# Optimization experiments

Measured on AMD Instinct MI355X. Metric: run time of the kernel, lower is better.

## Reference

```python
import jax, jax.numpy as jnp
import numpy as np

B, T, V, E, H, K = 64, 1024, 50000, 128, 256, 20
HD = H // 2  # hidden per LSTM direction


def _p(key, i, shape, scale=0.05):
    return jax.random.normal(jax.random.fold_in(key, i), shape, dtype=jnp.float32) * scale


def setup_inputs():
    key = jax.random.key(0)
    k1, k2, k3 = jax.random.split(key, 3)
    lengths = jax.random.randint(k2, (B,), T // 4, T + 1)
    mask = jnp.arange(T)[None, :] < lengths[:, None]  # [B,T] bool, left-aligned
    x = jax.random.randint(k1, (B, T), 1, V)
    x = jnp.where(mask, x, 0).astype(jnp.int32)  # pad_idx = 0
    tags = jax.random.randint(k3, (B, T), 0, K).astype(jnp.int32)
    inp = {"x": x, "tags": tags, "mask": mask}
    pk = jax.random.key(1)
    inp["emb"] = _p(pk, 0, (V, E)).at[0].set(0.0)  # padding_idx row zeroed
    dims = [E, H]  # layer-1 input is concat of both directions = H
    i = 1
    for l in range(2):
        for suf in ["", "_rev"]:
            inp[f"w_ih_l{l}{suf}"] = _p(pk, i, (4 * HD, dims[l])); i += 1
            inp[f"w_hh_l{l}{suf}"] = _p(pk, i, (4 * HD, HD)); i += 1
            inp[f"b_ih_l{l}{suf}"] = _p(pk, i, (4 * HD,)); i += 1
            inp[f"b_hh_l{l}{suf}"] = _p(pk, i, (4 * HD,)); i += 1
    inp["ln_g"] = jnp.ones((H,), jnp.float32)
    inp["ln_b"] = jnp.zeros((H,), jnp.float32)
    inp["attn_w"] = _p(pk, i, (1, H)); i += 1
    inp["attn_b"] = _p(pk, i, (1,)); i += 1
    inp["fc1_w"] = _p(pk, i, (H, H)); i += 1
    inp["fc1_b"] = _p(pk, i, (H,)); i += 1
    inp["fc2_w"] = _p(pk, i, (K, H)); i += 1
    inp["fc2_b"] = _p(pk, i, (K,)); i += 1
    inp["crf_start"] = _p(pk, i, (K,)); i += 1
    inp["crf_end"] = _p(pk, i, (K,)); i += 1
    inp["crf_trans"] = _p(pk, i, (K, K)); i += 1
    return inp


def _lstm_dir(x, w_ih, w_hh, b_ih, b_hh, reverse):
    # x: [B,T,D] -> [B,T,HD]; torch gate order i,f,g,o
    xs = jnp.swapaxes(x, 0, 1)  # [T,B,D]
    pre = xs @ w_ih.T + b_ih + b_hh  # input contribution precomputed (GEMM)

    def step(carry, g_in):
        h, c = carry
        g = g_in + h @ w_hh.T
        i, f, gc, o = jnp.split(g, 4, axis=-1)
        c = jax.nn.sigmoid(f) * c + jax.nn.sigmoid(i) * jnp.tanh(gc)
        h = jax.nn.sigmoid(o) * jnp.tanh(c)
        return (h, c), h

    nB, nH = x.shape[0], w_hh.shape[1]
    init = (jnp.zeros((nB, nH), x.dtype), jnp.zeros((nB, nH), x.dtype))
    _, hs = jax.lax.scan(step, init, pre, reverse=reverse)
    return jnp.swapaxes(hs, 0, 1)


def _crf_nll(emissions, tags, mask, start, end, trans):
    # torchcrf: llh = score - logZ, reduction='sum'; module returns -llh.mean() (scalar)
    maskf = mask.astype(emissions.dtype)
    em_sc = jnp.take_along_axis(emissions, tags[..., None], axis=2)[..., 0]  # [B,T]
    tr_sc = trans[tags[:, :-1], tags[:, 1:]]  # [B,T-1]
    num = start[tags[:, 0]] + em_sc[:, 0] + jnp.sum(maskf[:, 1:] * (tr_sc + em_sc[:, 1:]), axis=1)
    last = jnp.sum(mask.astype(jnp.int32), axis=1) - 1
    last_tags = jnp.take_along_axis(tags, last[:, None], axis=1)[:, 0]
    num = num + end[last_tags]
    alpha0 = start[None, :] + emissions[:, 0]  # [B,K]
    em_t = jnp.swapaxes(emissions[:, 1:], 0, 1)  # [T-1,B,K]
    m_t = jnp.swapaxes(mask[:, 1:], 0, 1)  # [T-1,B]

    def step(alpha, inp):
        e, m = inp
        nxt = jax.scipy.special.logsumexp(alpha[:, :, None] + trans[None] + e[:, None, :], axis=1)
        return jnp.where(m[:, None], nxt, alpha), None

    alpha, _ = jax.lax.scan(step, alpha0, (em_t, m_t))
    logZ = jax.scipy.special.logsumexp(alpha + end[None, :], axis=1)
    return -jnp.sum(num - logZ)


def reference(x, tags, mask, emb,
              w_ih_l0, w_hh_l0, b_ih_l0, b_hh_l0,
              w_ih_l0_rev, w_hh_l0_rev, b_ih_l0_rev, b_hh_l0_rev,
              w_ih_l1, w_hh_l1, b_ih_l1, b_hh_l1,
              w_ih_l1_rev, w_hh_l1_rev, b_ih_l1_rev, b_hh_l1_rev,
              ln_g, ln_b, attn_w, attn_b, fc1_w, fc1_b, fc2_w, fc2_b,
              crf_start, crf_end, crf_trans):
    mask = mask.at[:, 0].set(True)
    h = emb[x]  # [B,T,E]
    # 2-layer bidirectional LSTM (eval mode: dropout = identity)
    h = jnp.concatenate([
        _lstm_dir(h, w_ih_l0, w_hh_l0, b_ih_l0, b_hh_l0, False),
        _lstm_dir(h, w_ih_l0_rev, w_hh_l0_rev, b_ih_l0_rev, b_hh_l0_rev, True)], axis=-1)
    h = jnp.concatenate([
        _lstm_dir(h, w_ih_l1, w_hh_l1, b_ih_l1, b_hh_l1, False),
        _lstm_dir(h, w_ih_l1_rev, w_hh_l1_rev, b_ih_l1_rev, b_hh_l1_rev, True)], axis=-1)
    # LayerNorm (eps=1e-5)
    mu = jnp.mean(h, axis=-1, keepdims=True)
    var = jnp.mean(jnp.square(h - mu), axis=-1, keepdims=True)
    h = (h - mu) * jax.lax.rsqrt(var + 1e-5) * ln_g + ln_b
    # masked attention + residual broadcast of context
    scores = (h @ attn_w.T)[..., 0] + attn_b[0]  # [B,T]
    scores = jnp.where(mask, scores, jnp.float32(-1e9))
    w = jax.nn.softmax(scores, axis=1)[..., None]  # [B,T,1]
    h = h + jnp.sum(h * w, axis=1, keepdims=True)
    # hidden_fc: Linear + ReLU (dropout identity in eval)
    h = jax.nn.relu(h @ fc1_w.T + fc1_b)
    emissions = h @ fc2_w.T + fc2_b  # [B,T,K]
    return _crf_nll(emissions, tags, mask, crf_start, crf_end, crf_trans)
```

## Files before the change

kernel.cpp:

```cpp
#include <hip/hip_runtime.h>
#include <stdint.h>

#define BB 64
#define TT 1024
#define EE 128

typedef __bf16 bf16x8 __attribute__((ext_vector_type(8)));
typedef float f32x4 __attribute__((ext_vector_type(4)));

#define MFMA16 __builtin_amdgcn_mfma_f32_16x16x32_bf16

__device__ __forceinline__ float bf2f(unsigned short u) {
  union { unsigned int i; float f; } v; v.i = ((unsigned int)u) << 16; return v.f;
}
__device__ __forceinline__ unsigned short f2bf(float f) {
  union { float f; unsigned int i; } v; v.f = f;
  return (unsigned short)((v.i + 0x7fffu + ((v.i >> 16) & 1u)) >> 16);
}
__device__ __forceinline__ float sigf(float x) {
  return __builtin_amdgcn_rcpf(1.f + __expf(-x));
}
__device__ __forceinline__ float tanhf_(float x) {
  return fmaf(2.f, __builtin_amdgcn_rcpf(1.f + __expf(-2.f * x)), -1.f);
}


__global__ __launch_bounds__(256) void cvtbf4(const float* __restrict__ s,
                                              unsigned short* __restrict__ d, int n4) {
  int i = blockIdx.x * 256 + threadIdx.x;
  if (i < n4) {
    float4 v = *(const float4*)&s[(size_t)i * 4];
    ushort4 o; o.x = f2bf(v.x); o.y = f2bf(v.y); o.z = f2bf(v.z); o.w = f2bf(v.w);
    *(ushort4*)&d[(size_t)i * 4] = o;
  }
}

__global__ __launch_bounds__(256) void bias_comb(const float* bi, const float* bh,
                                                 const float* bir, const float* bhr,
                                                 float* __restrict__ o) {
  int j = blockIdx.x * 256 + threadIdx.x;
  if (j < 1024) o[j] = (j < 512) ? (bi[j] + bh[j]) : (bir[j - 512] + bhr[j - 512]);
}

__global__ __launch_bounds__(256) void embed_k(const int* __restrict__ x,
                                               const float* __restrict__ emb,
                                               unsigned short* __restrict__ xe) {
  int i = blockIdx.x * 256 + threadIdx.x;
  int bt = i >> 5, e4 = (i & 31) << 2;
  float4 v = *(const float4*)&emb[(size_t)x[bt] * EE + e4];
  ushort4 o; o.x = f2bf(v.x); o.y = f2bf(v.y); o.z = f2bf(v.z); o.w = f2bf(v.w);
  *(ushort4*)&xe[(size_t)bt * EE + e4] = o;
}


template <bool RELU, bool REMAP>
__global__ __launch_bounds__(256) void gemm_bt(const unsigned short* __restrict__ A,
                                               const unsigned short* __restrict__ W,
                                               const float* __restrict__ bias,
                                               unsigned short* __restrict__ out,
                                               int M, int N, int K) {
  __shared__ unsigned short As[64][40];
  __shared__ unsigned short Ws[64][40];
  const int tid = threadIdx.x, wave = tid >> 6, lane = tid & 63;
  const int m0 = blockIdx.x * 64, n0 = blockIdx.y * 64;
  f32x4 acc[4] = {{0,0,0,0},{0,0,0,0},{0,0,0,0},{0,0,0,0}};
  const int r = tid >> 2, kc = (tid & 3) << 3;
  const int fr = lane & 15, kk = (lane >> 4) << 3;

  for (int k0 = 0; k0 < K; k0 += 32) {
    uint4 av = *(const uint4*)&A[(size_t)(m0 + r) * K + k0 + kc];
    uint4 wv = *(const uint4*)&W[(size_t)(n0 + r) * K + k0 + kc];
    *(uint4*)&As[r][kc] = av;
    *(uint4*)&Ws[r][kc] = wv;
    __syncthreads();
    bf16x8 af = *(const bf16x8*)&As[wave * 16 + fr][kk];
#pragma unroll
    for (int nt = 0; nt < 4; nt++) {
      bf16x8 bv = *(const bf16x8*)&Ws[nt * 16 + fr][kk];
      acc[nt] = MFMA16(af, bv, acc[nt], 0, 0, 0);
    }
    __syncthreads();
  }
  const int cr = (lane >> 4) << 2, cc = lane & 15;
#pragma unroll
  for (int nt = 0; nt < 4; nt++) {
    int gn = n0 + nt * 16 + cc;
    float bs = bias[gn];
#pragma unroll
    for (int rr = 0; rr < 4; rr++) {
      int gm = m0 + wave * 16 + cr + rr;
      float v = acc[nt][rr] + bs;
      if (RELU) v = fmaxf(v, 0.f);
      size_t off;
      if (REMAP) { int b = gm >> 10, t = gm & 1023; off = ((size_t)(t * 64 + b)) * N + gn; }
      else       { off = (size_t)gm * N + gn; }
      out[off] = f2bf(v);
    }
  }
}


__global__ __launch_bounds__(512) void lstm_scan8(const unsigned short* __restrict__ pre,
                                                  const unsigned short* __restrict__ whhb,
                                                  unsigned short* __restrict__ hout) {
  const int b = blockIdx.x, dir = blockIdx.y;
  const int tid = threadIdx.x;
  const int w = tid >> 6, lane = tid & 63;
  const int fr = lane & 15, q = lane >> 4;
  const int u = 16 * w + fr;
  const unsigned short* wb = whhb + (size_t)dir * 65536;

  bf16x8 af[4][4];
#pragma unroll
  for (int G = 0; G < 4; G++)
#pragma unroll
    for (int kt = 0; kt < 4; kt++)
      af[G][kt] = *(const bf16x8*)&wb[(size_t)(128 * G + 16 * w + fr) * 128 + kt * 32 + q * 8];
  asm volatile("" : "+v"(af[0][0]), "+v"(af[0][1]), "+v"(af[0][2]), "+v"(af[0][3]),
                    "+v"(af[1][0]), "+v"(af[1][1]), "+v"(af[1][2]), "+v"(af[1][3]),
                    "+v"(af[2][0]), "+v"(af[2][1]), "+v"(af[2][2]), "+v"(af[2][3]),
                    "+v"(af[3][0]), "+v"(af[3][1]), "+v"(af[3][2]), "+v"(af[3][3]));

  __shared__ alignas(16) unsigned short hS[2][128];
  if (tid < 128) { hS[0][tid] = 0; hS[1][tid] = 0; }

  const int t0 = dir ? 1023 : 0, st = dir ? -1 : 1;
  float c = 0.f;
  const unsigned short* pb = pre + (size_t)b * 1024 + dir * 512 + u;
  unsigned short* hob = hout + (size_t)b * 1024 * 256 + dir * 128 + u;

  unsigned short pg0, pg1, pg2, pg3;
  {
    size_t tb = (size_t)t0 * 65536;
    pg0 = pb[tb]; pg1 = pb[tb + 128]; pg2 = pb[tb + 256]; pg3 = pb[tb + 384];
  }
  __syncthreads();

  int p = 0;
  for (int s = 0; s < 1024; s++) {
    const int t = t0 + st * s;
    bf16x8 bv0 = *(const bf16x8*)&hS[p][q * 8];
    bf16x8 bv1 = *(const bf16x8*)&hS[p][32 + q * 8];
    bf16x8 bv2 = *(const bf16x8*)&hS[p][64 + q * 8];
    bf16x8 bv3 = *(const bf16x8*)&hS[p][96 + q * 8];
    f32x4 c0 = {0,0,0,0}, c1 = {0,0,0,0}, c2 = {0,0,0,0}, c3 = {0,0,0,0};
    c0 = MFMA16(bv0, af[0][0], c0, 0,0,0); c1 = MFMA16(bv0, af[1][0], c1, 0,0,0);
    c2 = MFMA16(bv0, af[2][0], c2, 0,0,0); c3 = MFMA16(bv0, af[3][0], c3, 0,0,0);
    c0 = MFMA16(bv1, af[0][1], c0, 0,0,0); c1 = MFMA16(bv1, af[1][1], c1, 0,0,0);
    c2 = MFMA16(bv1, af[2][1], c2, 0,0,0); c3 = MFMA16(bv1, af[3][1], c3, 0,0,0);
    c0 = MFMA16(bv2, af[0][2], c0, 0,0,0); c1 = MFMA16(bv2, af[1][2], c1, 0,0,0);
    c2 = MFMA16(bv2, af[2][2], c2, 0,0,0); c3 = MFMA16(bv2, af[3][2], c3, 0,0,0);
    c0 = MFMA16(bv3, af[0][3], c0, 0,0,0); c1 = MFMA16(bv3, af[1][3], c1, 0,0,0);
    c2 = MFMA16(bv3, af[2][3], c2, 0,0,0); c3 = MFMA16(bv3, af[3][3], c3, 0,0,0);

    unsigned short ng0 = 0, ng1 = 0, ng2 = 0, ng3 = 0;
    if (s + 1 < 1024) {
      size_t tb = (size_t)(t + st) * 65536;
      ng0 = pb[tb]; ng1 = pb[tb + 128]; ng2 = pb[tb + 256]; ng3 = pb[tb + 384];
    }

    float gi = c0[0] + bf2f(pg0);
    float gf = c1[0] + bf2f(pg1);
    float gg = c2[0] + bf2f(pg2);
    float go = c3[0] + bf2f(pg3);
    float cn = sigf(gf) * c + sigf(gi) * tanhf_(gg);
    c = cn;
    float h = sigf(go) * tanhf_(cn);
    pg0 = ng0; pg1 = ng1; pg2 = ng2; pg3 = ng3;
    unsigned short hb = f2bf(h);
    if (q == 0) {
      hS[p ^ 1][u] = hb;
      hob[(size_t)t * 256] = hb;
    }
    asm volatile("s_waitcnt lgkmcnt(0)\n\ts_barrier" ::: "memory");
    p ^= 1;
  }
}


__global__ __launch_bounds__(256) void ln_attn(const unsigned short* __restrict__ h,
                                               const float* __restrict__ g,
                                               const float* __restrict__ be,
                                               const float* __restrict__ aw,
                                               const float* __restrict__ ab,
                                               float* __restrict__ hln,
                                               float* __restrict__ sc) {
  int row = blockIdx.x * 4 + (threadIdx.x >> 6);
  int lane = threadIdx.x & 63;
  ushort4 u = *(const ushort4*)&h[(size_t)row * 256 + lane * 4];
  float vx = bf2f(u.x), vy = bf2f(u.y), vz = bf2f(u.z), vw = bf2f(u.w);
  float s = vx + vy + vz + vw;
#pragma unroll
  for (int o = 1; o < 64; o <<= 1) s += __shfl_xor(s, o);
  float mu = s * (1.f / 256.f);
  float dx = vx - mu, dy = vy - mu, dz = vz - mu, dw = vw - mu;
  float q = dx * dx + dy * dy + dz * dz + dw * dw;
#pragma unroll
  for (int o = 1; o < 64; o <<= 1) q += __shfl_xor(q, o);
  float inv = rsqrtf(q * (1.f / 256.f) + 1e-5f);
  float4 gg = *(const float4*)&g[lane * 4];
  float4 bb = *(const float4*)&be[lane * 4];
  float y0 = dx * inv * gg.x + bb.x;
  float y1 = dy * inv * gg.y + bb.y;
  float y2 = dz * inv * gg.z + bb.z;
  float y3 = dw * inv * gg.w + bb.w;
  float4 ov; ov.x = y0; ov.y = y1; ov.z = y2; ov.w = y3;
  *(float4*)&hln[(size_t)row * 256 + lane * 4] = ov;
  float4 av = *(const float4*)&aw[lane * 4];
  float p = y0 * av.x + y1 * av.y + y2 * av.z + y3 * av.w;
#pragma unroll
  for (int o = 1; o < 64; o <<= 1) p += __shfl_xor(p, o);
  if (lane == 0) sc[row] = p + ab[0];
}


__global__ __launch_bounds__(256) void attn_pool(const float* __restrict__ scores,
                                                 const int* __restrict__ x,
                                                 const float* __restrict__ h_ln,
                                                 float* __restrict__ pooled) {
  int b = blockIdx.x, tid = threadIdx.x;
  __shared__ float wls[1024];
  __shared__ float red[4];
  float mx = -1e30f;
  for (int t = tid; t < 1024; t += 256) {
    bool valid = (t == 0) || (x[b * 1024 + t] != 0);
    float s = valid ? scores[b * 1024 + t] : -1e9f;
    wls[t] = s;
    mx = fmaxf(mx, s);
  }
#pragma unroll
  for (int o = 1; o < 64; o <<= 1) mx = fmaxf(mx, __shfl_xor(mx, o));
  if ((tid & 63) == 0) red[tid >> 6] = mx;
  __syncthreads();
  mx = fmaxf(fmaxf(red[0], red[1]), fmaxf(red[2], red[3]));
  __syncthreads();
  float sm = 0.f;
  for (int t = tid; t < 1024; t += 256) {
    float e = __expf(wls[t] - mx);
    wls[t] = e;
    sm += e;
  }
#pragma unroll
  for (int o = 1; o < 64; o <<= 1) sm += __shfl_xor(sm, o);
  if ((tid & 63) == 0) red[tid >> 6] = sm;
  __syncthreads();
  sm = red[0] + red[1] + red[2] + red[3];
  float inv = 1.f / sm;
  float a0 = 0.f, a1 = 0.f, a2 = 0.f, a3 = 0.f;
  const float* hb = h_ln + (size_t)b * 1024 * 256 + tid;
  for (int t = 0; t < 1024; t += 4) {
    a0 = fmaf(wls[t + 0], hb[(size_t)(t + 0) * 256], a0);
    a1 = fmaf(wls[t + 1], hb[(size_t)(t + 1) * 256], a1);
    a2 = fmaf(wls[t + 2], hb[(size_t)(t + 2) * 256], a2);
    a3 = fmaf(wls[t + 3], hb[(size_t)(t + 3) * 256], a3);
  }
  pooled[b * 256 + tid] = ((a0 + a1) + (a2 + a3)) * inv;
}

__global__ __launch_bounds__(256) void h2add(const float* __restrict__ h_ln,
                                             const float* __restrict__ pooled,
                                             unsigned short* __restrict__ h2) {
  size_t i = ((size_t)blockIdx.x * 256 + threadIdx.x) * 4;
  int b = (int)(i >> 18);
  int cidx = (int)(i & 255);
  float4 v = *(const float4*)&h_ln[i];
  float4 p = *(const float4*)&pooled[b * 256 + cidx];
  ushort4 o;
  o.x = f2bf(v.x + p.x); o.y = f2bf(v.y + p.y);
  o.z = f2bf(v.z + p.z); o.w = f2bf(v.w + p.w);
  *(ushort4*)&h2[i] = o;
}


__global__ __launch_bounds__(256) void fc2_emis(const unsigned short* __restrict__ fin,
                                                const float* __restrict__ w,
                                                const float* __restrict__ bias,
                                                float* __restrict__ em) {
  int row = blockIdx.x * 4 + (threadIdx.x >> 6);
  int lane = threadIdx.x & 63;
  ushort4 u = *(const ushort4*)&fin[(size_t)row * 256 + lane * 4];
  float x0 = bf2f(u.x), x1 = bf2f(u.y), x2 = bf2f(u.z), x3 = bf2f(u.w);
  float acc[20];
#pragma unroll
  for (int jj = 0; jj < 20; jj++) {
    float4 wv = *(const float4*)&w[jj * 256 + lane * 4];
    acc[jj] = x0 * wv.x + x1 * wv.y + x2 * wv.z + x3 * wv.w;
  }
#pragma unroll
  for (int jj = 0; jj < 20; jj++) {
#pragma unroll
    for (int o = 1; o < 64; o <<= 1) acc[jj] += __shfl_xor(acc[jj], o);
  }
  if (lane == 0) {
#pragma unroll
    for (int jj = 0; jj < 20; jj++) em[(size_t)row * 20 + jj] = acc[jj] + bias[jj];
  }
}


__global__ __launch_bounds__(64) void crf_k(const float* __restrict__ em,
                                            const int* __restrict__ tags,
                                            const int* __restrict__ x,
                                            const float* __restrict__ cs,
                                            const float* __restrict__ ce,
                                            const float* __restrict__ ctr,
                                            float* __restrict__ part) {
  int b = blockIdx.x, lane = threadIdx.x;
  const float* eb = em + (size_t)b * 1024 * 20;
  const int* tb = tags + b * 1024;
  const int* xb = x + b * 1024;

  int cnt = 0;
  for (int t = lane; t < 1024; t += 64) cnt += (t == 0 || xb[t] != 0) ? 1 : 0;
#pragma unroll
  for (int o = 1; o < 64; o <<= 1) cnt += __shfl_xor(cnt, o);
  int len = cnt;

  float ns = 0.f;
  for (int t = 1 + lane; t < len; t += 64)
    ns += ctr[tb[t - 1] * 20 + tb[t]] + eb[(size_t)t * 20 + tb[t]];
#pragma unroll
  for (int o = 1; o < 64; o <<= 1) ns += __shfl_xor(ns, o);
  float num = ns + cs[tb[0]] + eb[tb[0]] + ce[tb[len - 1]];

  __shared__ float al[32];
  if (lane < 32) al[lane] = (lane < 20) ? (cs[lane] + eb[lane]) : -1e30f;
  __syncthreads();

  int p = lane / 20, jj = lane % 20;
  int i0 = p * 7;
  float trc[7];
#pragma unroll
  for (int i = 0; i < 7; i++)
    trc[i] = (i0 + i < 20) ? ctr[(i0 + i) * 20 + jj] : -1e30f;

  for (int t = 1; t < len; t++) {
    float aa[7];
    float m = -3e30f;
#pragma unroll
    for (int i = 0; i < 7; i++) {
      float a = ((i0 + i < 28) ? al[i0 + i] : -1e30f) + trc[i];
      aa[i] = a;
      m = fmaxf(m, a);
    }
    float m0 = __shfl(m, jj), m1 = __shfl(m, jj + 20), m2 = __shfl(m, jj + 40);
    float mj = fmaxf(fmaxf(m0, m1), m2);
    float s = 0.f;
#pragma unroll
    for (int i = 0; i < 7; i++) s += __expf(aa[i] - mj);
    float s0 = __shfl(s, jj), s1 = __shfl(s, jj + 20), s2 = __shfl(s, jj + 40);
    float na = mj + __logf(s0 + s1 + s2) + eb[(size_t)t * 20 + jj];
    __syncthreads();
    if (lane < 20) al[lane] = na;
    __syncthreads();
  }

  float v = (lane < 20) ? (al[lane] + ce[lane]) : -3e30f;
  float mm = v;
#pragma unroll
  for (int o = 1; o < 64; o <<= 1) mm = fmaxf(mm, __shfl_xor(mm, o));
  float ss = (lane < 20) ? __expf(v - mm) : 0.f;
#pragma unroll
  for (int o = 1; o < 64; o <<= 1) ss += __shfl_xor(ss, o);
  float logZ = mm + __logf(ss);
  if (lane == 0) part[b] = logZ - num;
}

__global__ __launch_bounds__(64) void finalsum(const float* __restrict__ part,
                                               float* __restrict__ out) {
  float v = part[threadIdx.x];
#pragma unroll
  for (int o = 1; o < 64; o <<= 1) v += __shfl_xor(v, o);
  if (threadIdx.x == 0) out[0] = v;
}


extern "C" void kernel_launch(void* const* d_in, const int* in_sizes, int n_in,
                              void* d_out, int out_size, void* d_ws, size_t ws_size,
                              hipStream_t stream) {
  (void)in_sizes; (void)n_in; (void)out_size; (void)ws_size;
  const int*   x     = (const int*)  d_in[0];
  const int*   tags  = (const int*)  d_in[1];
  const float* emb   = (const float*)d_in[3];
  const float* wih0  = (const float*)d_in[4];
  const float* whh0  = (const float*)d_in[5];
  const float* bih0  = (const float*)d_in[6];
  const float* bhh0  = (const float*)d_in[7];
  const float* wih0r = (const float*)d_in[8];
  const float* whh0r = (const float*)d_in[9];
  const float* bih0r = (const float*)d_in[10];
  const float* bhh0r = (const float*)d_in[11];
  const float* wih1  = (const float*)d_in[12];
  const float* whh1  = (const float*)d_in[13];
  const float* bih1  = (const float*)d_in[14];
  const float* bhh1  = (const float*)d_in[15];
  const float* wih1r = (const float*)d_in[16];
  const float* whh1r = (const float*)d_in[17];
  const float* bih1r = (const float*)d_in[18];
  const float* bhh1r = (const float*)d_in[19];
  const float* lng   = (const float*)d_in[20];
  const float* lnb   = (const float*)d_in[21];
  const float* attw  = (const float*)d_in[22];
  const float* attb  = (const float*)d_in[23];
  const float* fc1w  = (const float*)d_in[24];
  const float* fc1b  = (const float*)d_in[25];
  const float* fc2w  = (const float*)d_in[26];
  const float* fc2b  = (const float*)d_in[27];
  const float* cst   = (const float*)d_in[28];
  const float* cen   = (const float*)d_in[29];
  const float* ctr   = (const float*)d_in[30];

  char* base = (char*)d_ws;
  const size_t MB = 1024 * 1024;

  unsigned short* PRE  = (unsigned short*)(base);
  float*          HLN  = (float*)(base);
  unsigned short* H2   = (unsigned short*)(base + 64 * MB);
  unsigned short* FC1O = (unsigned short*)(base + 96 * MB);
  unsigned short* XEMB = (unsigned short*)(base + 128 * MB);
  unsigned short* HL0  = (unsigned short*)(base + 128 * MB);
  unsigned short* HL1  = (unsigned short*)(base + 128 * MB);
  float*          EM   = (float*)(base + 128 * MB);
  char* sm = base + 160 * MB;
  unsigned short* WIH0  = (unsigned short*)sm;  sm += (size_t)2 * 512 * 128 * 2;
  unsigned short* WIH1  = (unsigned short*)sm;  sm += (size_t)2 * 512 * 256 * 2;
  unsigned short* FC1W  = (unsigned short*)sm;  sm += (size_t)256 * 256 * 2;
  unsigned short* WHHB0 = (unsigned short*)sm;  sm += (size_t)2 * 512 * 128 * 2;
  unsigned short* WHHB1 = (unsigned short*)sm;  sm += (size_t)2 * 512 * 128 * 2;
  float* BIAS0 = (float*)sm; sm += 1024 * 4;
  float* BIAS1 = (float*)sm; sm += 1024 * 4;
  float* SCORE = (float*)sm; sm += (size_t)BB * TT * 4;
  float* POOL  = (float*)sm; sm += 64 * 256 * 4;
  float* PART  = (float*)sm; sm += 256;

  cvtbf4<<<64, 256, 0, stream>>>(wih0, WIH0, 65536 / 4);
  cvtbf4<<<64, 256, 0, stream>>>(wih0r, WIH0 + 65536, 65536 / 4);
  cvtbf4<<<128, 256, 0, stream>>>(wih1, WIH1, 131072 / 4);
  cvtbf4<<<128, 256, 0, stream>>>(wih1r, WIH1 + 131072, 131072 / 4);
  cvtbf4<<<64, 256, 0, stream>>>(fc1w, FC1W, 65536 / 4);
  cvtbf4<<<64, 256, 0, stream>>>(whh0, WHHB0, 65536 / 4);
  cvtbf4<<<64, 256, 0, stream>>>(whh0r, WHHB0 + 65536, 65536 / 4);
  cvtbf4<<<64, 256, 0, stream>>>(whh1, WHHB1, 65536 / 4);
  cvtbf4<<<64, 256, 0, stream>>>(whh1r, WHHB1 + 65536, 65536 / 4);
  bias_comb<<<4, 256, 0, stream>>>(bih0, bhh0, bih0r, bhh0r, BIAS0);
  bias_comb<<<4, 256, 0, stream>>>(bih1, bhh1, bih1r, bhh1r, BIAS1);

  embed_k<<<8192, 256, 0, stream>>>(x, emb, XEMB);

  gemm_bt<false, true><<<dim3(1024, 16), 256, 0, stream>>>(XEMB, WIH0, BIAS0, PRE, 65536, 1024, 128);
  lstm_scan8<<<dim3(64, 2), 512, 0, stream>>>(PRE, WHHB0, HL0);

  gemm_bt<false, true><<<dim3(1024, 16), 256, 0, stream>>>(HL0, WIH1, BIAS1, PRE, 65536, 1024, 256);
  lstm_scan8<<<dim3(64, 2), 512, 0, stream>>>(PRE, WHHB1, HL1);

  ln_attn<<<16384, 256, 0, stream>>>(HL1, lng, lnb, attw, attb, HLN, SCORE);
  attn_pool<<<64, 256, 0, stream>>>(SCORE, x, HLN, POOL);
  h2add<<<16384, 256, 0, stream>>>(HLN, POOL, H2);

  gemm_bt<true, false><<<dim3(1024, 4), 256, 0, stream>>>(H2, FC1W, fc1b, FC1O, 65536, 256, 256);
  fc2_emis<<<16384, 256, 0, stream>>>(FC1O, fc2w, fc2b, EM);

  crf_k<<<64, 64, 0, stream>>>(EM, tags, x, cst, cen, ctr, PART);
  finalsum<<<1, 64, 0, stream>>>(PART, (float*)d_out);
}
```

Baseline: 1.793 ms.

## Stage GEMM output through LDS, unroll LSTM scan by two, store LN output as bf16

The GEMM epilogue now writes results into a shared-memory tile and then issues 16-byte vectorized global stores, replacing scattered 2-byte stores. The LSTM recurrence is unrolled by two steps so each pre-activation load is issued two steps ahead, giving more latency slack. The LayerNorm output buffer is stored as bf16 instead of fp32, which halves traffic in ln_attn, attn_pool and h2add. The bf16 storage adds rounding to the LayerNorm activations, and the extra LDS tile raises shared memory use per GEMM block.

Measured after the change: 1.709 ms. 1.05x faster.

```diff
diff --git a/kernel.cpp b/kernel.cpp
--- a/kernel.cpp
+++ b/kernel.cpp
@@ -61,6 +61,7 @@
                                                int M, int N, int K) {
   __shared__ unsigned short As[64][40];
   __shared__ unsigned short Ws[64][40];
+  __shared__ unsigned short Cs[64][72];
   const int tid = threadIdx.x, wave = tid >> 6, lane = tid & 63;
   const int m0 = blockIdx.x * 64, n0 = blockIdx.y * 64;
   f32x4 acc[4] = {{0,0,0,0},{0,0,0,0},{0,0,0,0},{0,0,0,0}};
@@ -84,25 +85,58 @@
   const int cr = (lane >> 4) << 2, cc = lane & 15;
 #pragma unroll
   for (int nt = 0; nt < 4; nt++) {
-    int gn = n0 + nt * 16 + cc;
-    float bs = bias[gn];
+    float bs = bias[n0 + nt * 16 + cc];
 #pragma unroll
     for (int rr = 0; rr < 4; rr++) {
-      int gm = m0 + wave * 16 + cr + rr;
       float v = acc[nt][rr] + bs;
       if (RELU) v = fmaxf(v, 0.f);
-      size_t off;
-      if (REMAP) { int b = gm >> 10, t = gm & 1023; off = ((size_t)(t * 64 + b)) * N + gn; }
-      else       { off = (size_t)gm * N + gn; }
-      out[off] = f2bf(v);
+      Cs[wave * 16 + cr + rr][nt * 16 + cc] = f2bf(v);
     }
   }
-}
-
-
-__global__ __launch_bounds__(512) void lstm_scan8(const unsigned short* __restrict__ pre,
-                                                  const unsigned short* __restrict__ whhb,
-                                                  unsigned short* __restrict__ hout) {
+  __syncthreads();
+  const int row = tid >> 2, c0 = (tid & 3) * 16;
+  uint4 v0 = *(const uint4*)&Cs[row][c0];
+  uint4 v1 = *(const uint4*)&Cs[row][c0 + 8];
+  const int gm = m0 + row;
+  size_t off;
+  if (REMAP) { int b = gm >> 10, t = gm & 1023; off = ((size_t)(t * 64 + b)) * N + n0 + c0; }
+  else       { off = (size_t)gm * N + n0 + c0; }
+  *(uint4*)&out[off] = v0;
+  *(uint4*)&out[off + 8] = v1;
+}
+
+
+#define SCAN_STEP10(PG0, PG1, PG2, PG3, TIDX) {                               \
+    bf16x8 bv0 = *(const bf16x8*)&hS[p][q * 8];                               \
+    bf16x8 bv1 = *(const bf16x8*)&hS[p][32 + q * 8];                          \
+    bf16x8 bv2 = *(const bf16x8*)&hS[p][64 + q * 8];                          \
+    bf16x8 bv3 = *(const bf16x8*)&hS[p][96 + q * 8];                          \
+    f32x4 c0 = {0,0,0,0}, c1 = {0,0,0,0}, c2 = {0,0,0,0}, c3 = {0,0,0,0};     \
+    c0 = MFMA16(bv0, af[0][0], c0, 0,0,0); c1 = MFMA16(bv0, af[1][0], c1, 0,0,0); \
+    c2 = MFMA16(bv0, af[2][0], c2, 0,0,0); c3 = MFMA16(bv0, af[3][0], c3, 0,0,0); \
+    c0 = MFMA16(bv1, af[0][1], c0, 0,0,0); c1 = MFMA16(bv1, af[1][1], c1, 0,0,0); \
+    c2 = MFMA16(bv1, af[2][1], c2, 0,0,0); c3 = MFMA16(bv1, af[3][1], c3, 0,0,0); \
+    c0 = MFMA16(bv2, af[0][2], c0, 0,0,0); c1 = MFMA16(bv2, af[1][2], c1, 0,0,0); \
+    c2 = MFMA16(bv2, af[2][2], c2, 0,0,0); c3 = MFMA16(bv2, af[3][2], c3, 0,0,0); \
+    c0 = MFMA16(bv3, af[0][3], c0, 0,0,0); c1 = MFMA16(bv3, af[1][3], c1, 0,0,0); \
+    c2 = MFMA16(bv3, af[2][3], c2, 0,0,0); c3 = MFMA16(bv3, af[3][3], c3, 0,0,0); \
+    float gi = c0[0] + bf2f(PG0);                                             \
+    float gf = c1[0] + bf2f(PG1);                                             \
+    float gg = c2[0] + bf2f(PG2);                                             \
+    float go = c3[0] + bf2f(PG3);                                             \
+    float cn = sigf(gf) * c + sigf(gi) * tanhf_(gg);                          \
+    c = cn;                                                                   \
+    float h = sigf(go) * tanhf_(cn);                                          \
+    unsigned short hb_ = f2bf(h);                                             \
+    if (q == 0) {                                                             \
+      hS[p ^ 1][u] = hb_;                                                     \
+      hob[(size_t)(TIDX) * 256] = hb_;                   \
+    }                                                                         \
+  }
+
+__global__ __launch_bounds__(512) void lstm_scan10(const unsigned short* __restrict__ pre,
+                                                   const unsigned short* __restrict__ whhb,
+                                                   unsigned short* __restrict__ hout) {
   const int b = blockIdx.x, dir = blockIdx.y;
   const int tid = threadIdx.x;
   const int w = tid >> 6, lane = tid & 63;
@@ -129,48 +163,29 @@
   const unsigned short* pb = pre + (size_t)b * 1024 + dir * 512 + u;
   unsigned short* hob = hout + (size_t)b * 1024 * 256 + dir * 128 + u;
 
-  unsigned short pg0, pg1, pg2, pg3;
+  unsigned short pA0, pA1, pA2, pA3, pB0, pB1, pB2, pB3;
   {
     size_t tb = (size_t)t0 * 65536;
-    pg0 = pb[tb]; pg1 = pb[tb + 128]; pg2 = pb[tb + 256]; pg3 = pb[tb + 384];
+    pA0 = pb[tb]; pA1 = pb[tb + 128]; pA2 = pb[tb + 256]; pA3 = pb[tb + 384];
+    tb = (size_t)(t0 + st) * 65536;
+    pB0 = pb[tb]; pB1 = pb[tb + 128]; pB2 = pb[tb + 256]; pB3 = pb[tb + 384];
   }
   __syncthreads();
 
   int p = 0;
-  for (int s = 0; s < 1024; s++) {
+  for (int s = 0; s < 1024; s += 2) {
     const int t = t0 + st * s;
-    bf16x8 bv0 = *(const bf16x8*)&hS[p][q * 8];
-    bf16x8 bv1 = *(const bf16x8*)&hS[p][32 + q * 8];
-    bf16x8 bv2 = *(const bf16x8*)&hS[p][64 + q * 8];
-    bf16x8 bv3 = *(const bf16x8*)&hS[p][96 + q * 8];
-    f32x4 c0 = {0,0,0,0}, c1 = {0,0,0,0}, c2 = {0,0,0,0}, c3 = {0,0,0,0};
-    c0 = MFMA16(bv0, af[0][0], c0, 0,0,0); c1 = MFMA16(bv0, af[1][0], c1, 0,0,0);
-    c2 = MFMA16(bv0, af[2][0], c2, 0,0,0); c3 = MFMA16(bv0, af[3][0], c3, 0,0,0);
-    c0 = MFMA16(bv1, af[0][1], c0, 0,0,0); c1 = MFMA16(bv1, af[1][1], c1, 0,0,0);
-    c2 = MFMA16(bv1, af[2][1], c2, 0,0,0); c3 = MFMA16(bv1, af[3][1], c3, 0,0,0);
-    c0 = MFMA16(bv2, af[0][2], c0, 0,0,0); c1 = MFMA16(bv2, af[1][2], c1, 0,0,0);
-    c2 = MFMA16(bv2, af[2][2], c2, 0,0,0); c3 = MFMA16(bv2, af[3][2], c3, 0,0,0);
-    c0 = MFMA16(bv3, af[0][3], c0, 0,0,0); c1 = MFMA16(bv3, af[1][3], c1, 0,0,0);
-    c2 = MFMA16(bv3, af[2][3], c2, 0,0,0); c3 = MFMA16(bv3, af[3][3], c3, 0,0,0);
-
-    unsigned short ng0 = 0, ng1 = 0, ng2 = 0, ng3 = 0;
-    if (s + 1 < 1024) {
-      size_t tb = (size_t)(t + st) * 65536;
-      ng0 = pb[tb]; ng1 = pb[tb + 128]; ng2 = pb[tb + 256]; ng3 = pb[tb + 384];
+    SCAN_STEP10(pA0, pA1, pA2, pA3, t)
+    if (s + 2 < 1024) {
+      size_t tb = (size_t)(t0 + st * (s + 2)) * 65536;
+      pA0 = pb[tb]; pA1 = pb[tb + 128]; pA2 = pb[tb + 256]; pA3 = pb[tb + 384];
     }
-
-    float gi = c0[0] + bf2f(pg0);
-    float gf = c1[0] + bf2f(pg1);
-    float gg = c2[0] + bf2f(pg2);
-    float go = c3[0] + bf2f(pg3);
-    float cn = sigf(gf) * c + sigf(gi) * tanhf_(gg);
-    c = cn;
-    float h = sigf(go) * tanhf_(cn);
-    pg0 = ng0; pg1 = ng1; pg2 = ng2; pg3 = ng3;
-    unsigned short hb = f2bf(h);
-    if (q == 0) {
-      hS[p ^ 1][u] = hb;
-      hob[(size_t)t * 256] = hb;
+    asm volatile("s_waitcnt lgkmcnt(0)\n\ts_barrier" ::: "memory");
+    p ^= 1;
+    SCAN_STEP10(pB0, pB1, pB2, pB3, t + st)
+    if (s + 3 < 1024) {
+      size_t tb = (size_t)(t0 + st * (s + 3)) * 65536;
+      pB0 = pb[tb]; pB1 = pb[tb + 128]; pB2 = pb[tb + 256]; pB3 = pb[tb + 384];
     }
     asm volatile("s_waitcnt lgkmcnt(0)\n\ts_barrier" ::: "memory");
     p ^= 1;
@@ -183,7 +198,7 @@
                                                const float* __restrict__ be,
                                                const float* __restrict__ aw,
                                                const float* __restrict__ ab,
-                                               float* __restrict__ hln,
+                                               unsigned short* __restrict__ hln,
                                                float* __restrict__ sc) {
   int row = blockIdx.x * 4 + (threadIdx.x >> 6);
   int lane = threadIdx.x & 63;
@@ -204,8 +219,8 @@
   float y1 = dy * inv * gg.y + bb.y;
   float y2 = dz * inv * gg.z + bb.z;
   float y3 = dw * inv * gg.w + bb.w;
-  float4 ov; ov.x = y0; ov.y = y1; ov.z = y2; ov.w = y3;
-  *(float4*)&hln[(size_t)row * 256 + lane * 4] = ov;
+  ushort4 ov; ov.x = f2bf(y0); ov.y = f2bf(y1); ov.z = f2bf(y2); ov.w = f2bf(y3);
+  *(ushort4*)&hln[(size_t)row * 256 + lane * 4] = ov;
   float4 av = *(const float4*)&aw[lane * 4];
   float p = y0 * av.x + y1 * av.y + y2 * av.z + y3 * av.w;
 #pragma unroll
@@ -216,7 +231,7 @@
 
 __global__ __launch_bounds__(256) void attn_pool(const float* __restrict__ scores,
                                                  const int* __restrict__ x,
-                                                 const float* __restrict__ h_ln,
+                                                 const unsigned short* __restrict__ h_ln,
                                                  float* __restrict__ pooled) {
   int b = blockIdx.x, tid = threadIdx.x;
   __shared__ float wls[1024];
@@ -247,27 +262,27 @@
   sm = red[0] + red[1] + red[2] + red[3];
   float inv = 1.f / sm;
   float a0 = 0.f, a1 = 0.f, a2 = 0.f, a3 = 0.f;
-  const float* hb = h_ln + (size_t)b * 1024 * 256 + tid;
+  const unsigned short* hb = h_ln + (size_t)b * 1024 * 256 + tid;
   for (int t = 0; t < 1024; t += 4) {
-    a0 = fmaf(wls[t + 0], hb[(size_t)(t + 0) * 256], a0);
-    a1 = fmaf(wls[t + 1], hb[(size_t)(t + 1) * 256], a1);
-    a2 = fmaf(wls[t + 2], hb[(size_t)(t + 2) * 256], a2);
-    a3 = fmaf(wls[t + 3], hb[(size_t)(t + 3) * 256], a3);
+    a0 = fmaf(wls[t + 0], bf2f(hb[(size_t)(t + 0) * 256]), a0);
+    a1 = fmaf(wls[t + 1], bf2f(hb[(size_t)(t + 1) * 256]), a1);
+    a2 = fmaf(wls[t + 2], bf2f(hb[(size_t)(t + 2) * 256]), a2);
+    a3 = fmaf(wls[t + 3], bf2f(hb[(size_t)(t + 3) * 256]), a3);
   }
   pooled[b * 256 + tid] = ((a0 + a1) + (a2 + a3)) * inv;
 }
 
-__global__ __launch_bounds__(256) void h2add(const float* __restrict__ h_ln,
+__global__ __launch_bounds__(256) void h2add(const unsigned short* __restrict__ h_ln,
                                              const float* __restrict__ pooled,
                                              unsigned short* __restrict__ h2) {
   size_t i = ((size_t)blockIdx.x * 256 + threadIdx.x) * 4;
   int b = (int)(i >> 18);
   int cidx = (int)(i & 255);
-  float4 v = *(const float4*)&h_ln[i];
+  ushort4 v = *(const ushort4*)&h_ln[i];
   float4 p = *(const float4*)&pooled[b * 256 + cidx];
   ushort4 o;
-  o.x = f2bf(v.x + p.x); o.y = f2bf(v.y + p.y);
-  o.z = f2bf(v.z + p.z); o.w = f2bf(v.w + p.w);
+  o.x = f2bf(bf2f(v.x) + p.x); o.y = f2bf(bf2f(v.y) + p.y);
+  o.z = f2bf(bf2f(v.z) + p.z); o.w = f2bf(bf2f(v.w) + p.w);
   *(ushort4*)&h2[i] = o;
 }
 
@@ -414,7 +429,7 @@
   const size_t MB = 1024 * 1024;
 
   unsigned short* PRE  = (unsigned short*)(base);
-  float*          HLN  = (float*)(base);
+  unsigned short* HLN  = (unsigned short*)(base);
   unsigned short* H2   = (unsigned short*)(base + 64 * MB);
   unsigned short* FC1O = (unsigned short*)(base + 96 * MB);
   unsigned short* XEMB = (unsigned short*)(base + 128 * MB);
@@ -448,10 +463,10 @@
   embed_k<<<8192, 256, 0, stream>>>(x, emb, XEMB);
 
   gemm_bt<false, true><<<dim3(1024, 16), 256, 0, stream>>>(XEMB, WIH0, BIAS0, PRE, 65536, 1024, 128);
-  lstm_scan8<<<dim3(64, 2), 512, 0, stream>>>(PRE, WHHB0, HL0);
+  lstm_scan10<<<dim3(64, 2), 512, 0, stream>>>(PRE, WHHB0, HL0);
 
   gemm_bt<false, true><<<dim3(1024, 16), 256, 0, stream>>>(HL0, WIH1, BIAS1, PRE, 65536, 1024, 256);
-  lstm_scan8<<<dim3(64, 2), 512, 0, stream>>>(PRE, WHHB1, HL1);
+  lstm_scan10<<<dim3(64, 2), 512, 0, stream>>>(PRE, WHHB1, HL1);
 
   ln_attn<<<16384, 256, 0, stream>>>(HL1, lng, lnb, attw, attb, HLN, SCORE);
   attn_pool<<<64, 256, 0, stream>>>(SCORE, x, HLN, POOL);
```
